# Kernel optimization log

Hardware: AMD Instinct MI355X
Metric: run time of the kernel (lower is better)

Reference implementation:

```python
import jax, jax.numpy as jnp
import numpy as np
import itertools

B, N, K, G = 1024, 1024, 6, 720  # G = K!
H1, H2, C = 64, 32, 40
IN = K * 3


def setup_inputs() -> dict:
    key = jax.random.key(0)
    ks = jax.random.split(key, 8)
    x = jax.random.normal(ks[0], (B, N, 3), dtype=jnp.float32)
    # per-sample subsample indices (torch uses randperm(N)[:K]; distinctness
    # is irrelevant to the math, randint keeps them in-range)
    idx = jax.random.randint(ks[1], (B, K), 0, N)
    perms = jnp.asarray(
        np.array(list(itertools.permutations(range(K))), dtype=np.int32)
    )  # (G, K)
    # MLP params: torch Linear default init ~ U(-1/sqrt(fan_in), 1/sqrt(fan_in))
    def lin(k, fin, fout):
        kw, kb = jax.random.split(k)
        s = 1.0 / np.sqrt(fin)
        W = jax.random.uniform(kw, (fin, fout), jnp.float32, -s, s)
        b = jax.random.uniform(kb, (fout,), jnp.float32, -s, s)
        return W, b
    W1, b1 = lin(ks[2], IN, H1)
    W2, b2 = lin(ks[3], H1, H2)
    W3, b3 = lin(ks[4], H2, C)
    return dict(x=x, W1=W1, b1=b1, W2=W2, b2=b2, W3=W3, b3=b3,
                idx=idx, perms=perms)


def reference(x, W1, b1, W2, b2, W3, b3, idx, perms):
    Bv = x.shape[0]
    Gv, Kv = perms.shape
    # gather the K subsampled points per batch element: (B, K, 3)
    pts = jnp.take_along_axis(x, idx[:, :, None], axis=1)
    # expand over all K! permutations of the point ordering: (B, G, K, 3)
    permuted = pts[:, perms, :]
    flat = permuted.reshape(Bv, Gv, Kv * 3)  # (B, G, K*3)
    h = jax.nn.relu(flat @ W1 + b1)          # (B, G, H1)
    h = jax.nn.relu(h @ W2 + b2)             # (B, G, H2)
    y = h @ W3 + b3                          # (B, G, C)
    return y.mean(axis=1)                    # (B, C)
```

## Files before the change

### kernel.cpp

```cpp
#include <hip/hip_runtime.h>
#include <hip/hip_bf16.h>

typedef __attribute__((ext_vector_type(8))) short short8;
typedef __attribute__((ext_vector_type(4))) float f32x4;

#define NN 1024

#define LFENCE { asm volatile("s_waitcnt lgkmcnt(0)" ::: "memory"); __builtin_amdgcn_sched_barrier(0); }

#define ROW_W(ROW, VAL) { \
  float v_ = fmaxf((VAL), 0.0f); \
  __hip_bfloat16 hb_ = __float2bfloat16(v_); \
  h1s[((ROW) * 64) + (lane ^ ((((ROW)) & 7) << 3))] = *(short*)&hb_; \
}

#define ROW6(R, BX) \
  ROW_W((R)+0,(BX)+T0_) ROW_W((R)+1,(BX)+T1_) ROW_W((R)+2,(BX)+T2_) \
  ROW_W((R)+3,(BX)+T3_) ROW_W((R)+4,(BX)+T4_) ROW_W((R)+5,(BX)+T5_)

#define SGR(R0, A0,A1,A2, M0,M1,M2) do { \
  const float f0_ = b1v + P[(A0)*6+0]; \
  const float f1_ = b1v + P[(A1)*6+0]; \
  const float f2_ = b1v + P[(A2)*6+0]; \
  const float g12_ = P[(A1)*6+1] + P[(A2)*6+2]; \
  const float g21_ = P[(A2)*6+1] + P[(A1)*6+2]; \
  const float g02_ = P[(A0)*6+1] + P[(A2)*6+2]; \
  const float g20_ = P[(A2)*6+1] + P[(A0)*6+2]; \
  const float g01_ = P[(A0)*6+1] + P[(A1)*6+2]; \
  const float g10_ = P[(A1)*6+1] + P[(A0)*6+2]; \
  const float e0_ = P[(M0)*6+3], e1_ = P[(M1)*6+3], e2_ = P[(M2)*6+3]; \
  const float h12_ = P[(M1)*6+4] + P[(M2)*6+5]; \
  const float h21_ = P[(M2)*6+4] + P[(M1)*6+5]; \
  const float h02_ = P[(M0)*6+4] + P[(M2)*6+5]; \
  const float h20_ = P[(M2)*6+4] + P[(M0)*6+5]; \
  const float h01_ = P[(M0)*6+4] + P[(M1)*6+5]; \
  const float h10_ = P[(M1)*6+4] + P[(M0)*6+5]; \
  const float T0_ = e0_+h12_, T1_ = e0_+h21_, T2_ = e1_+h02_; \
  const float T3_ = e1_+h20_, T4_ = e2_+h01_, T5_ = e2_+h10_; \
  const float B0_ = f0_+g12_, B1_ = f0_+g21_, B2_ = f1_+g02_; \
  const float B3_ = f1_+g20_, B4_ = f2_+g01_, B5_ = f2_+g10_; \
  ROW6((R0)+0,  B0_) ROW6((R0)+6,  B1_) ROW6((R0)+12, B2_) \
  ROW6((R0)+18, B3_) ROW6((R0)+24, B4_) ROW6((R0)+30, B5_) \
} while(0)

#define MFMA8(A0_, A1_) do { \
  f32x4 c0_ = {b2v0,b2v0,b2v0,b2v0}; \
  f32x4 c1_ = {b2v1,b2v1,b2v1,b2v1}; \
  c0_ = __builtin_amdgcn_mfma_f32_16x16x32_bf16(A0_, bh00, c0_, 0,0,0); \
  c0_ = __builtin_amdgcn_mfma_f32_16x16x32_bf16(A1_, bh10, c0_, 0,0,0); \
  c0_ = __builtin_amdgcn_mfma_f32_16x16x32_bf16(A0_, bl00, c0_, 0,0,0); \
  c0_ = __builtin_amdgcn_mfma_f32_16x16x32_bf16(A1_, bl10, c0_, 0,0,0); \
  c1_ = __builtin_amdgcn_mfma_f32_16x16x32_bf16(A0_, bh01, c1_, 0,0,0); \
  c1_ = __builtin_amdgcn_mfma_f32_16x16x32_bf16(A1_, bh11, c1_, 0,0,0); \
  c1_ = __builtin_amdgcn_mfma_f32_16x16x32_bf16(A0_, bl01, c1_, 0,0,0); \
  c1_ = __builtin_amdgcn_mfma_f32_16x16x32_bf16(A1_, bl11, c1_, 0,0,0); \
  acc0[0]+=fmaxf(c0_[0],0.f); acc0[1]+=fmaxf(c0_[1],0.f); \
  acc0[2]+=fmaxf(c0_[2],0.f); acc0[3]+=fmaxf(c0_[3],0.f); \
  acc1[0]+=fmaxf(c1_[0],0.f); acc1[1]+=fmaxf(c1_[1],0.f); \
  acc1[2]+=fmaxf(c1_[2],0.f); acc1[3]+=fmaxf(c1_[3],0.f); \
} while(0)

#define PHASEB do { \
  LFENCE; \
  _Pragma("unroll") \
  for (int t_ = 0; t_ < 9; ++t_) { \
    short8 A0_ = *(const short8*)&h1s[t_ * 1024 + e0i]; \
    short8 A1_ = *(const short8*)&h1s[t_ * 1024 + e1i]; \
    MFMA8(A0_, A1_); \
  } \
} while(0)

#define MKB(dst_h, dst_l, KH, NIDX) do { \
  _Pragma("unroll") \
  for (int e_ = 0; e_ < 8; ++e_) { \
    float f_ = W2[((KH)*32 + kg*8 + e_)*32 + 16*(NIDX) + colb]; \
    __hip_bfloat16 hi_ = __float2bfloat16(f_); \
    float lof_ = f_ - __bfloat162float(hi_); \
    __hip_bfloat16 lo_ = __float2bfloat16(lof_); \
    dst_h[e_] = *(short*)&hi_; dst_l[e_] = *(short*)&lo_; \
  } \
} while(0)

__global__ __launch_bounds__(64, 1) void symm_mlp_kernel(
    const float* __restrict__ x,
    const float* __restrict__ W1, const float* __restrict__ b1,
    const float* __restrict__ W2, const float* __restrict__ b2,
    const float* __restrict__ W3, const float* __restrict__ b3,
    const int* __restrict__ idx, const int* __restrict__ perms,
    float* __restrict__ out)
{
    __shared__ short h1s[144 * 64];

    const int lane  = threadIdx.x;
    const int batch = blockIdx.x;

    float w1c[18];
    #pragma unroll
    for (int r = 0; r < 18; ++r) w1c[r] = W1[r * 64 + lane];

    float px[6][3];
    #pragma unroll
    for (int k = 0; k < 6; ++k) {
        int p = idx[batch * 6 + k];
        #pragma unroll
        for (int d = 0; d < 3; ++d) px[k][d] = x[(batch * NN + p) * 3 + d];
    }

    float P[36];
    #pragma unroll
    for (int k = 0; k < 6; ++k)
    #pragma unroll
    for (int j = 0; j < 6; ++j)
        P[k*6+j] = fmaf(px[k][2], w1c[3*j+2], fmaf(px[k][1], w1c[3*j+1], px[k][0] * w1c[3*j+0]));

    const float b1v = b1[lane];

    const int colb = lane & 15, kg = lane >> 4;
    short8 bh00, bl00, bh10, bl10, bh01, bl01, bh11, bl11;
    MKB(bh00, bl00, 0, 0);
    MKB(bh10, bl10, 1, 0);
    MKB(bh01, bl01, 0, 1);
    MKB(bh11, bl11, 1, 1);
    const float b2v0 = b2[colb];
    const float b2v1 = b2[16 + colb];

    const int Xl  = (lane & 7) << 3;
    const int e0i = (lane & 15) * 64 + ((kg * 8) ^ Xl);
    const int e1i = (lane & 15) * 64 + ((32 + kg * 8) ^ Xl);

    f32x4 acc0 = {0.f,0.f,0.f,0.f}, acc1 = {0.f,0.f,0.f,0.f};

    SGR(0,   0,1,2, 3,4,5);  SGR(36,  0,1,3, 2,4,5);
    SGR(72,  0,1,4, 2,3,5);  SGR(108, 0,1,5, 2,3,4);
    PHASEB;
    SGR(0,   0,2,3, 1,4,5);  SGR(36,  0,2,4, 1,3,5);
    SGR(72,  0,2,5, 1,3,4);  SGR(108, 0,3,4, 1,2,5);
    PHASEB;
    SGR(0,   0,3,5, 1,2,4);  SGR(36,  0,4,5, 1,2,3);
    SGR(72,  1,2,3, 0,4,5);  SGR(108, 1,2,4, 0,3,5);
    PHASEB;
    SGR(0,   1,2,5, 0,3,4);  SGR(36,  1,3,4, 0,2,5);
    SGR(72,  1,3,5, 0,2,4);  SGR(108, 1,4,5, 0,2,3);
    PHASEB;
    SGR(0,   2,3,4, 0,1,5);  SGR(36,  2,3,5, 0,1,4);
    SGR(72,  2,4,5, 0,1,3);  SGR(108, 3,4,5, 0,1,2);
    PHASEB;

    float s0 = acc0[0] + acc0[1] + acc0[2] + acc0[3];
    float s1 = acc1[0] + acc1[1] + acc1[2] + acc1[3];
    s0 += __shfl_xor(s0, 16, 64);  s0 += __shfl_xor(s0, 32, 64);
    s1 += __shfl_xor(s1, 16, 64);  s1 += __shfl_xor(s1, 32, 64);

    float* wf = reinterpret_cast<float*>(h1s);
    if (lane < 32) wf[lane] = (lane < 16 ? s0 : s1) * (1.0f / 720.0f);
    LFENCE;

    if (lane < 40) {
        float y = b3[lane];
        #pragma unroll
        for (int c = 0; c < 32; ++c) y = fmaf(wf[c], W3[c * 40 + lane], y);
        out[batch * 40 + lane] = y;
    }
}

extern "C" void kernel_launch(void* const* d_in, const int* in_sizes, int n_in,
                              void* d_out, int out_size, void* d_ws, size_t ws_size,
                              hipStream_t stream) {
    const float* x  = (const float*)d_in[0];
    const float* W1 = (const float*)d_in[1];
    const float* b1 = (const float*)d_in[2];
    const float* W2 = (const float*)d_in[3];
    const float* b2 = (const float*)d_in[4];
    const float* W3 = (const float*)d_in[5];
    const float* b3 = (const float*)d_in[6];
    const int* idx   = (const int*)d_in[7];
    const int* perms = (const int*)d_in[8];
    (void)perms;
    float* out = (float*)d_out;

    symm_mlp_kernel<<<1024, 64, 0, stream>>>(x, W1, b1, W2, b2, W3, b3, idx, perms, out);
}
```

Baseline: 21.47 us.

## Split permutation groups across four wavefronts per batch with padded per-wave chunks

Each block now runs four wavefronts, and each wave handles five of the twenty 36-row permutation groups. A wave writes each group into its own 48-row LDS buffer and runs three MFMA tiles on it. The 12 zero-padded rows give relu(b2) rows, and their contribution is subtracted afterwards. Partial sums are combined through shared memory with a barrier before the final W3 projection. This raises parallelism per batch, at the cost of 25% padded MFMA work and a block-level sync, and every wave recomputes the P and B-fragment setup.

Result: slower. 39.97 us (+86.2%).

```diff
diff --git a/kernel.cpp b/kernel.cpp
--- a/kernel.cpp
+++ b/kernel.cpp
@@ -3,6 +3,8 @@
 
 typedef __attribute__((ext_vector_type(8))) short short8;
 typedef __attribute__((ext_vector_type(4))) float f32x4;
+typedef __attribute__((ext_vector_type(4))) unsigned int u32x4;
+typedef __attribute__((ext_vector_type(2))) unsigned int u32x2;
 
 #define NN 1024
 
@@ -11,14 +13,14 @@
 #define ROW_W(ROW, VAL) { \
   float v_ = fmaxf((VAL), 0.0f); \
   __hip_bfloat16 hb_ = __float2bfloat16(v_); \
-  h1s[((ROW) * 64) + (lane ^ ((((ROW)) & 7) << 3))] = *(short*)&hb_; \
+  wb[((ROW) * 64) + (lane ^ ((((ROW)) & 7) << 3))] = *(short*)&hb_; \
 }
 
 #define ROW6(R, BX) \
   ROW_W((R)+0,(BX)+T0_) ROW_W((R)+1,(BX)+T1_) ROW_W((R)+2,(BX)+T2_) \
   ROW_W((R)+3,(BX)+T3_) ROW_W((R)+4,(BX)+T4_) ROW_W((R)+5,(BX)+T5_)
 
-#define SGR(R0, A0,A1,A2, M0,M1,M2) do { \
+#define SGR(A0,A1,A2, M0,M1,M2) do { \
   const float f0_ = b1v + P[(A0)*6+0]; \
   const float f1_ = b1v + P[(A1)*6+0]; \
   const float f2_ = b1v + P[(A2)*6+0]; \
@@ -39,8 +41,8 @@
   const float T3_ = e1_+h20_, T4_ = e2_+h01_, T5_ = e2_+h10_; \
   const float B0_ = f0_+g12_, B1_ = f0_+g21_, B2_ = f1_+g02_; \
   const float B3_ = f1_+g20_, B4_ = f2_+g01_, B5_ = f2_+g10_; \
-  ROW6((R0)+0,  B0_) ROW6((R0)+6,  B1_) ROW6((R0)+12, B2_) \
-  ROW6((R0)+18, B3_) ROW6((R0)+24, B4_) ROW6((R0)+30, B5_) \
+  ROW6(0,  B0_) ROW6(6,  B1_) ROW6(12, B2_) \
+  ROW6(18, B3_) ROW6(24, B4_) ROW6(30, B5_) \
 } while(0)
 
 #define MFMA8(A0_, A1_) do { \
@@ -60,15 +62,17 @@
   acc1[2]+=fmaxf(c1_[2],0.f); acc1[3]+=fmaxf(c1_[3],0.f); \
 } while(0)
 
-#define PHASEB do { \
+#define PHASEB3 do { \
   LFENCE; \
   _Pragma("unroll") \
-  for (int t_ = 0; t_ < 9; ++t_) { \
-    short8 A0_ = *(const short8*)&h1s[t_ * 1024 + e0i]; \
-    short8 A1_ = *(const short8*)&h1s[t_ * 1024 + e1i]; \
+  for (int t_ = 0; t_ < 3; ++t_) { \
+    short8 A0_ = *(const short8*)&wb[t_ * 1024 + e0i]; \
+    short8 A1_ = *(const short8*)&wb[t_ * 1024 + e1i]; \
     MFMA8(A0_, A1_); \
   } \
 } while(0)
+
+#define CH1(A0,A1,A2, M0,M1,M2) do { SGR(A0,A1,A2, M0,M1,M2); PHASEB3; } while(0)
 
 #define MKB(dst_h, dst_l, KH, NIDX) do { \
   _Pragma("unroll") \
@@ -81,7 +85,7 @@
   } \
 } while(0)
 
-__global__ __launch_bounds__(64, 1) void symm_mlp_kernel(
+__global__ __launch_bounds__(256, 4) void symm_mlp_kernel(
     const float* __restrict__ x,
     const float* __restrict__ W1, const float* __restrict__ b1,
     const float* __restrict__ W2, const float* __restrict__ b2,
@@ -89,30 +93,33 @@
     const int* __restrict__ idx, const int* __restrict__ perms,
     float* __restrict__ out)
 {
-    __shared__ short h1s[144 * 64];
+    __shared__ short h1s[4][48 * 64];
+    __shared__ float redbuf[4][32];
 
-    const int lane  = threadIdx.x;
+    const int tid   = threadIdx.x;
+    const int lane  = tid & 63;
+    const int wv    = tid >> 6;
     const int batch = blockIdx.x;
 
-    float w1c[18];
-    #pragma unroll
-    for (int r = 0; r < 18; ++r) w1c[r] = W1[r * 64 + lane];
+    float P[36];
+    {
+        float w1c[18];
+        #pragma unroll
+        for (int r = 0; r < 18; ++r) w1c[r] = W1[r * 64 + lane];
 
-    float px[6][3];
-    #pragma unroll
-    for (int k = 0; k < 6; ++k) {
-        int p = idx[batch * 6 + k];
+        float px[6][3];
         #pragma unroll
-        for (int d = 0; d < 3; ++d) px[k][d] = x[(batch * NN + p) * 3 + d];
+        for (int k = 0; k < 6; ++k) {
+            int p = idx[batch * 6 + k];
+            #pragma unroll
+            for (int d = 0; d < 3; ++d) px[k][d] = x[(batch * NN + p) * 3 + d];
+        }
+        #pragma unroll
+        for (int k = 0; k < 6; ++k)
+        #pragma unroll
+        for (int j = 0; j < 6; ++j)
+            P[k*6+j] = fmaf(px[k][2], w1c[3*j+2], fmaf(px[k][1], w1c[3*j+1], px[k][0] * w1c[3*j+0]));
     }
-
-    float P[36];
-    #pragma unroll
-    for (int k = 0; k < 6; ++k)
-    #pragma unroll
-    for (int j = 0; j < 6; ++j)
-        P[k*6+j] = fmaf(px[k][2], w1c[3*j+2], fmaf(px[k][1], w1c[3*j+1], px[k][0] * w1c[3*j+0]));
-
     const float b1v = b1[lane];
 
     const int colb = lane & 15, kg = lane >> 4;
@@ -124,42 +131,50 @@
     const float b2v0 = b2[colb];
     const float b2v1 = b2[16 + colb];
 
+    short* wb = &h1s[wv][0];
+    *reinterpret_cast<u32x4*>(&wb[2304 + lane * 8]) = u32x4{0u, 0u, 0u, 0u};
+    *reinterpret_cast<u32x2*>(&wb[2816 + lane * 4]) = u32x2{0u, 0u};
+
     const int Xl  = (lane & 7) << 3;
     const int e0i = (lane & 15) * 64 + ((kg * 8) ^ Xl);
     const int e1i = (lane & 15) * 64 + ((32 + kg * 8) ^ Xl);
 
     f32x4 acc0 = {0.f,0.f,0.f,0.f}, acc1 = {0.f,0.f,0.f,0.f};
 
-    SGR(0,   0,1,2, 3,4,5);  SGR(36,  0,1,3, 2,4,5);
-    SGR(72,  0,1,4, 2,3,5);  SGR(108, 0,1,5, 2,3,4);
-    PHASEB;
-    SGR(0,   0,2,3, 1,4,5);  SGR(36,  0,2,4, 1,3,5);
-    SGR(72,  0,2,5, 1,3,4);  SGR(108, 0,3,4, 1,2,5);
-    PHASEB;
-    SGR(0,   0,3,5, 1,2,4);  SGR(36,  0,4,5, 1,2,3);
-    SGR(72,  1,2,3, 0,4,5);  SGR(108, 1,2,4, 0,3,5);
-    PHASEB;
-    SGR(0,   1,2,5, 0,3,4);  SGR(36,  1,3,4, 0,2,5);
-    SGR(72,  1,3,5, 0,2,4);  SGR(108, 1,4,5, 0,2,3);
-    PHASEB;
-    SGR(0,   2,3,4, 0,1,5);  SGR(36,  2,3,5, 0,1,4);
-    SGR(72,  2,4,5, 0,1,3);  SGR(108, 3,4,5, 0,1,2);
-    PHASEB;
+    if (wv == 0) {
+        CH1(0,1,2, 3,4,5);  CH1(0,1,3, 2,4,5);  CH1(0,1,4, 2,3,5);
+        CH1(0,1,5, 2,3,4);  CH1(0,2,3, 1,4,5);
+    } else if (wv == 1) {
+        CH1(0,2,4, 1,3,5);  CH1(0,2,5, 1,3,4);  CH1(0,3,4, 1,2,5);
+        CH1(0,3,5, 1,2,4);  CH1(0,4,5, 1,2,3);
+    } else if (wv == 2) {
+        CH1(1,2,3, 0,4,5);  CH1(1,2,4, 0,3,5);  CH1(1,2,5, 0,3,4);
+        CH1(1,3,4, 0,2,5);  CH1(1,3,5, 0,2,4);
+    } else {
+        CH1(1,4,5, 0,2,3);  CH1(2,3,4, 0,1,5);  CH1(2,3,5, 0,1,4);
+        CH1(2,4,5, 0,1,3);  CH1(3,4,5, 0,1,2);
+    }
 
     float s0 = acc0[0] + acc0[1] + acc0[2] + acc0[3];
     float s1 = acc1[0] + acc1[1] + acc1[2] + acc1[3];
     s0 += __shfl_xor(s0, 16, 64);  s0 += __shfl_xor(s0, 32, 64);
     s1 += __shfl_xor(s1, 16, 64);  s1 += __shfl_xor(s1, 32, 64);
+    s0 -= 60.0f * fmaxf(b2v0, 0.0f);
+    s1 -= 60.0f * fmaxf(b2v1, 0.0f);
 
-    float* wf = reinterpret_cast<float*>(h1s);
-    if (lane < 32) wf[lane] = (lane < 16 ? s0 : s1) * (1.0f / 720.0f);
-    LFENCE;
+    if (lane < 16)       redbuf[wv][lane]      = s0;
+    else if (lane < 32)  redbuf[wv][lane]      = s1;
+    __syncthreads();
 
-    if (lane < 40) {
-        float y = b3[lane];
+    if (tid < 40) {
+        float m[32];
         #pragma unroll
-        for (int c = 0; c < 32; ++c) y = fmaf(wf[c], W3[c * 40 + lane], y);
-        out[batch * 40 + lane] = y;
+        for (int c = 0; c < 32; ++c)
+            m[c] = (redbuf[0][c] + redbuf[1][c] + redbuf[2][c] + redbuf[3][c]) * (1.0f / 720.0f);
+        float y = b3[tid];
+        #pragma unroll
+        for (int c = 0; c < 32; ++c) y = fmaf(m[c], W3[c * 40 + tid], y);
+        out[batch * 40 + tid] = y;
     }
 }
 
@@ -178,5 +193,5 @@
     (void)perms;
     float* out = (float*)d_out;
 
-    symm_mlp_kernel<<<1024, 64, 0, stream>>>(x, W1, b1, W2, b2, W3, b3, idx, perms, out);
+    symm_mlp_kernel<<<1024, 256, 0, stream>>>(x, W1, b1, W2, b2, W3, b3, idx, perms, out);
 }
```
